# Performance work log

Measured on AMD Instinct MI355X. Metric: run time of the kernel, lower is better.

The kernel has to match this reference:

```python
import jax, jax.numpy as jnp
import numpy as np

B = 4           # batchsize == poolsize, pool = arange(B)
N_NODES = 32768
N_EDGES = 262144
CH_V = 16
CH_E = 16
HID = 64
CH_MSG = 2 * CH_V + CH_E  # 48


def setup_inputs() -> dict:
    key = jax.random.key(0)
    ks = jax.random.split(key, 8)
    node_vals = jax.random.normal(ks[0], (B, N_NODES, CH_V), jnp.float32) * 0.01
    edge_vals = jax.random.normal(ks[1], (B, N_EDGES, CH_E), jnp.float32) * 0.1
    conn_a = jax.random.randint(ks[2], (N_EDGES,), 0, N_NODES)
    conn_b = jax.random.randint(ks[3], (N_EDGES,), 0, N_NODES)
    w = lambda k, sh: jax.random.normal(k, sh, jnp.float32) * 0.1
    return {
        "node_vals": node_vals, "edge_vals": edge_vals,
        "conn_a": conn_a, "conn_b": conn_b,
        "Wm1": w(ks[4], (CH_MSG, HID)), "bm1": jnp.zeros((HID,), jnp.float32),
        "Wm2": w(ks[5], (HID, CH_MSG)), "bm2": jnp.zeros((CH_MSG,), jnp.float32),
        "Wu1": w(ks[6], (3 * CH_V, HID)), "bu1": jnp.zeros((HID,), jnp.float32),
        "Wu2": w(ks[7], (HID, CH_V)), "bu2": jnp.zeros((CH_V,), jnp.float32),
    }


def reference(node_vals, edge_vals, conn_a, conn_b,
              Wm1, bm1, Wm2, bm2, Wu1, bu1, Wu2, bu2):
    # NeuralGraph.timestep with node_dropout_p = edge_dropout_p = 0 (masks are identity),
    # use_update=True, average_messages=True, nodes=True, edges=True.
    h_a = node_vals[:, conn_a]                      # [B, E, CH_V] gather at source nodes
    h_b = node_vals[:, conn_b]                      # [B, E, CH_V] gather at target nodes
    h = jnp.concatenate([h_a, h_b, edge_vals], -1)  # [B, E, 48]
    # message MLP (Linear -> tanh -> Linear)
    m = jnp.tanh(h @ Wm1 + bm1) @ Wm2 + bm2         # [B, E, 48]
    m_a = m[..., :CH_V]
    m_b = m[..., CH_V:2 * CH_V]
    m_ab = m[..., 2 * CH_V:]
    # scatter-add aggregation per node (index_add_ along node dim)
    agg_a = jnp.zeros((B, N_NODES, CH_V), m.dtype).at[:, conn_a].add(m_a)
    agg_b = jnp.zeros((B, N_NODES, CH_V), m.dtype).at[:, conn_b].add(m_b)
    # count-based averaging (counts clamped to >= 1, matching the buffer fixup)
    ones = jnp.ones((N_EDGES,), m.dtype)
    cnt_a = jnp.maximum(jax.ops.segment_sum(ones, conn_a, num_segments=N_NODES), 1.0)
    cnt_b = jnp.maximum(jax.ops.segment_sum(ones, conn_b, num_segments=N_NODES), 1.0)
    agg_a = agg_a / cnt_a[None, :, None]
    agg_b = agg_b / cnt_b[None, :, None]
    # update MLP
    u_in = jnp.concatenate([agg_a, agg_b, node_vals], -1)   # [B, N, 48]
    updates = jnp.tanh(u_in @ Wu1 + bu1) @ Wu2 + bu2        # [B, N, CH_V]
    new_node_vals = node_vals + updates
    new_edge_vals = edge_vals + m_ab
    return new_node_vals, new_edge_vals
```

## Files before the change

kernel.cpp:

```cpp
#include <hip/hip_runtime.h>
#include <hip/hip_bf16.h>
#include <cstdint>
#include <cstddef>

#define B 4
#define NN 32768
#define NE 262144
#define CV 16
#define CE 16
#define HID 64
#define CM 48

using frag  = __attribute__((ext_vector_type(8))) short;
using f32x4 = __attribute__((ext_vector_type(4))) float;

__device__ __forceinline__ float fast_tanh(float x) {
    float e = __expf(2.0f * x);
    return 1.0f - 2.0f / (e + 1.0f);
}

__device__ __forceinline__ unsigned short f2bf(float x) {
    union { float f; unsigned u; } v; v.f = x;
    unsigned r = (v.u + 0x7FFFu + ((v.u >> 16) & 1u)) >> 16;
    return (unsigned short)r;
}

__device__ __forceinline__ float bf2f(unsigned short x) {
    union { unsigned u; float f; } v; v.u = ((unsigned)x) << 16;
    return v.f;
}

__device__ __forceinline__ unsigned pk2bf(float lo, float hi) {
    union { __hip_bfloat162 h; unsigned u; } v;
    v.h = __float22bfloat162_rn(make_float2(lo, hi));
    return v.u;
}

__device__ __forceinline__ unsigned swo(int row, int byte_off) {
    return (unsigned)((row << 7) + (byte_off ^ ((row & 7) << 4)));
}

__device__ __forceinline__ void acc8(float* a, uint4 v) {
    a[0] += bf2f((unsigned short)(v.x & 0xFFFFu));
    a[1] += bf2f((unsigned short)(v.x >> 16));
    a[2] += bf2f((unsigned short)(v.y & 0xFFFFu));
    a[3] += bf2f((unsigned short)(v.y >> 16));
    a[4] += bf2f((unsigned short)(v.z & 0xFFFFu));
    a[5] += bf2f((unsigned short)(v.z >> 16));
    a[6] += bf2f((unsigned short)(v.w & 0xFFFFu));
    a[7] += bf2f((unsigned short)(v.w >> 16));
}

__global__ __launch_bounds__(256) void count_kernel(
    const int* __restrict__ ca, const int* __restrict__ cb,
    int* __restrict__ cnt_a, int* __restrict__ cnt_b,
    int* __restrict__ rank_a, int* __restrict__ rank_b,
    const float* __restrict__ Wm1, const float* __restrict__ bm1,
    const float* __restrict__ Wm2,
    const float* __restrict__ Wu1, const float* __restrict__ bu1,
    const float* __restrict__ Wu2,
    const float* __restrict__ node_vals,
    unsigned short* __restrict__ pW1, unsigned short* __restrict__ pW2,
    unsigned short* __restrict__ pWu1, unsigned short* __restrict__ pWu2,
    unsigned short* __restrict__ nv16)
{
    int i = blockIdx.x * 256 + threadIdx.x;
    rank_a[i] = atomicAdd(&cnt_a[ca[i]], 1);
    rank_b[i] = atomicAdd(&cnt_b[cb[i]], 1);

    {
        int x0 = i * 8;
        const float4* src = (const float4*)(node_vals + x0);
        float4 v0 = src[0], v1 = src[1];
        uint4 o;
        o.x = pk2bf(v0.x, v0.y); o.y = pk2bf(v0.z, v0.w);
        o.z = pk2bf(v1.x, v1.y); o.w = pk2bf(v1.z, v1.w);
        *(uint4*)(nv16 + x0) = o;
    }

    if (blockIdx.x == 0) {
        for (int x = threadIdx.x; x < 4 * 2 * 64 * 8; x += 256) {
            int j = x & 7, lane = (x >> 3) & 63, ks = (x >> 9) & 1, mt = x >> 10;
            int m = mt * 16 + (lane & 15);
            int k = ks * 32 + (lane >> 4) * 8 + j;
            float w = (k < 48) ? Wm1[k * 64 + m] : (k == 48 ? bm1[m] : 0.0f);
            pW1[x] = f2bf(w);
        }
    } else if (blockIdx.x == 1) {
        for (int x = threadIdx.x; x < 3 * 2 * 64 * 8; x += 256) {
            int j = x & 7, lane = (x >> 3) & 63, ks = (x >> 9) & 1, mt = x >> 10;
            int m = mt * 16 + (lane & 15);
            int k = ks * 32 + (lane >> 4) * 8 + j;
            pW2[x] = f2bf(Wm2[k * 48 + m]);
        }
    } else if (blockIdx.x == 2) {
        for (int x = threadIdx.x; x < 4 * 2 * 64 * 8; x += 256) {
            int j = x & 7, lane = (x >> 3) & 63, ks = (x >> 9) & 1, mt = x >> 10;
            int m = mt * 16 + (lane & 15);
            int k = ks * 32 + (lane >> 4) * 8 + j;
            float w = (k < 48) ? Wu1[k * 64 + m] : (k == 48 ? bu1[m] : 0.0f);
            pWu1[x] = f2bf(w);
        }
    } else if (blockIdx.x == 3) {
        for (int x = threadIdx.x; x < 2 * 64 * 8; x += 256) {
            int j = x & 7, lane = (x >> 3) & 63, ks = x >> 9;
            int m = lane & 15;
            int k = ks * 32 + (lane >> 4) * 8 + j;
            pWu2[x] = f2bf(Wu2[k * 16 + m]);
        }
    }
}

__global__ __launch_bounds__(1024) void scan_kernel(
    const int* __restrict__ cnt_a, int* __restrict__ start_a,
    const int* __restrict__ cnt_b, int* __restrict__ start_b)
{
    const int* cnt = (blockIdx.x == 0) ? cnt_a : cnt_b;
    int* start     = (blockIdx.x == 0) ? start_a : start_b;

    __shared__ int sw[16];
    int t = threadIdx.x;
    int lane = t & 63;
    int wv   = t >> 6;
    int base = t * 32;

    int local[32];
    int sum = 0;
    const int4* p = (const int4*)(cnt + base);
#pragma unroll
    for (int q = 0; q < 8; q++) {
        int4 v = p[q];
        local[q*4+0] = v.x; local[q*4+1] = v.y; local[q*4+2] = v.z; local[q*4+3] = v.w;
        sum += v.x + v.y + v.z + v.w;
    }
    int inc = sum;
#pragma unroll
    for (int off = 1; off < 64; off <<= 1) {
        int u = __shfl_up(inc, off);
        if (lane >= off) inc += u;
    }
    if (lane == 63) sw[wv] = inc;
    __syncthreads();
    if (wv == 0 && lane < 16) {
        int v = sw[lane];
        int i2 = v;
#pragma unroll
        for (int off = 1; off < 16; off <<= 1) {
            int u = __shfl_up(i2, off);
            if (lane >= off) i2 += u;
        }
        sw[lane] = i2 - v;
    }
    __syncthreads();

    int run = sw[wv] + inc - sum;
    int4* ps = (int4*)(start + base);
#pragma unroll
    for (int q = 0; q < 8; q++) {
        int4 o;
        o.x = run; run += local[q*4+0];
        o.y = run; run += local[q*4+1];
        o.z = run; run += local[q*4+2];
        o.w = run; run += local[q*4+3];
        ps[q] = o;
    }
}

__global__ __launch_bounds__(256, 5) void edge_kernel(
    const unsigned short* __restrict__ nv16, const float* __restrict__ edge_vals,
    const int* __restrict__ ca, const int* __restrict__ cb,
    const int* __restrict__ rank_a, const int* __restrict__ rank_b,
    const int* __restrict__ start_a, const int* __restrict__ start_b,
    const unsigned short* __restrict__ pW1, const unsigned short* __restrict__ pW2,
    const float* __restrict__ bm2,
    float* __restrict__ out_edge,
    unsigned short* __restrict__ ma_csr, unsigned short* __restrict__ mb_csr)
{
    __shared__ unsigned short sH[256 * 64];
    char* sB = (char*)sH;

    int t    = threadIdx.x;
    int lane = t & 63;
    int col  = lane & 15;
    int quad = lane >> 4;
    int erow = (t >> 6) * 64;

    size_t eb  = (size_t)blockIdx.x * 256;
    size_t idx = eb + t;
    int e  = (int)(idx & (NE - 1));
    int bb = (int)(idx >> 18);

    int na = ca[e], nb = cb[e];
    int posx = start_a[na] + rank_a[e];
    int posy = start_b[nb] + rank_b[e];

    float4 ev[4];
    {
        const uint4* gA = (const uint4*)(nv16 + ((size_t)bb * NN + na) * CV);
        const uint4* gB = (const uint4*)(nv16 + ((size_t)bb * NN + nb) * CV);
        uint4 a0 = gA[0], a1 = gA[1];
        uint4 b0 = gB[0], b1 = gB[1];
        const float4* pE = (const float4*)(edge_vals + idx * CE);
#pragma unroll
        for (int q = 0; q < 4; q++) ev[q] = pE[q];

        unsigned pk[32];
        *(uint4*)&pk[0]  = a0;  *(uint4*)&pk[4]  = a1;
        *(uint4*)&pk[8]  = b0;  *(uint4*)&pk[12] = b1;
#pragma unroll
        for (int q = 0; q < 4; q++) {
            pk[16 + 2*q + 0] = pk2bf(ev[q].x, ev[q].y);
            pk[16 + 2*q + 1] = pk2bf(ev[q].z, ev[q].w);
        }
        pk[24] = 0x3F80u;
#pragma unroll
        for (int q = 25; q < 32; q++) pk[q] = 0;
        const uint4* src = (const uint4*)pk;
#pragma unroll
        for (int q = 0; q < 8; q++)
            *(uint4*)(sB + swo(t, q * 16)) = src[q];
    }
    asm volatile("s_waitcnt lgkmcnt(0)" ::: "memory");

#pragma unroll
    for (int hh = 0; hh < 2; hh++) {
        int r0 = erow + hh * 32 + col;

        frag w1f[4][2];
#pragma unroll
        for (int mt = 0; mt < 4; mt++)
#pragma unroll
            for (int ks = 0; ks < 2; ks++)
                w1f[mt][ks] = *(const frag*)&pW1[(((mt * 2 + ks) * 64) + lane) * 8];

        f32x4 acc1[4][2];
#pragma unroll
        for (int mt = 0; mt < 4; mt++)
#pragma unroll
            for (int n = 0; n < 2; n++) acc1[mt][n] = (f32x4){0.f, 0.f, 0.f, 0.f};

#pragma unroll
        for (int ks = 0; ks < 2; ks++) {
            frag bfr[2];
#pragma unroll
            for (int n = 0; n < 2; n++)
                bfr[n] = *(const frag*)(sB + swo(r0 + n * 16, ks * 64 + quad * 16));
#pragma unroll
            for (int mt = 0; mt < 4; mt++)
#pragma unroll
                for (int n = 0; n < 2; n++)
                    acc1[mt][n] = __builtin_amdgcn_mfma_f32_16x16x32_bf16(
                        w1f[mt][ks], bfr[n], acc1[mt][n], 0, 0, 0);
        }

#pragma unroll
        for (int n = 0; n < 2; n++) {
            int row = r0 + n * 16;
#pragma unroll
            for (int mt = 0; mt < 4; mt++) {
                uint2 w;
                w.x = pk2bf(fast_tanh(acc1[mt][n][0]), fast_tanh(acc1[mt][n][1]));
                w.y = pk2bf(fast_tanh(acc1[mt][n][2]), fast_tanh(acc1[mt][n][3]));
                *(uint2*)(sB + swo(row, mt * 32 + quad * 8)) = w;
            }
        }
        asm volatile("s_waitcnt lgkmcnt(0)" ::: "memory");

        frag w2f[3][2];
#pragma unroll
        for (int mt = 0; mt < 3; mt++)
#pragma unroll
            for (int ks = 0; ks < 2; ks++)
                w2f[mt][ks] = *(const frag*)&pW2[(((mt * 2 + ks) * 64) + lane) * 8];

        f32x4 acc2[3][2];
#pragma unroll
        for (int mt = 0; mt < 3; mt++)
#pragma unroll
            for (int n = 0; n < 2; n++) acc2[mt][n] = (f32x4){0.f, 0.f, 0.f, 0.f};

#pragma unroll
        for (int ks = 0; ks < 2; ks++) {
            frag bfr[2];
#pragma unroll
            for (int n = 0; n < 2; n++)
                bfr[n] = *(const frag*)(sB + swo(r0 + n * 16, ks * 64 + quad * 16));
#pragma unroll
            for (int mt = 0; mt < 3; mt++)
#pragma unroll
                for (int n = 0; n < 2; n++)
                    acc2[mt][n] = __builtin_amdgcn_mfma_f32_16x16x32_bf16(
                        w2f[mt][ks], bfr[n], acc2[mt][n], 0, 0, 0);
        }

#pragma unroll
        for (int n = 0; n < 2; n++) {
            int row = r0 + n * 16;
            float4 v;
            v.x = acc2[2][n][0]; v.y = acc2[2][n][1];
            v.z = acc2[2][n][2]; v.w = acc2[2][n][3];
            *(float4*)(sB + swo(row, 64 + quad * 16)) = v;
        }

        float4 b2a = *(const float4*)&bm2[quad * 4];
        float4 b2b = *(const float4*)&bm2[16 + quad * 4];
#pragma unroll
        for (int n = 0; n < 2; n++) {
            int row = r0 + n * 16;
            uint2 wa;
            wa.x = pk2bf(acc2[0][n][0] + b2a.x, acc2[0][n][1] + b2a.y);
            wa.y = pk2bf(acc2[0][n][2] + b2a.z, acc2[0][n][3] + b2a.w);
            *(uint2*)(sB + swo(row, quad * 8)) = wa;
            uint2 wb;
            wb.x = pk2bf(acc2[1][n][0] + b2b.x, acc2[1][n][1] + b2b.y);
            wb.y = pk2bf(acc2[1][n][2] + b2b.z, acc2[1][n][3] + b2b.w);
            *(uint2*)(sB + swo(row, 32 + quad * 8)) = wb;
        }
    }
    asm volatile("s_waitcnt lgkmcnt(0)" ::: "memory");

    {
        uint4 a0 = *(const uint4*)(sB + swo(t, 0));
        uint4 a1 = *(const uint4*)(sB + swo(t, 16));
        uint4 b0 = *(const uint4*)(sB + swo(t, 32));
        uint4 b1 = *(const uint4*)(sB + swo(t, 48));
        unsigned short* pa = &ma_csr[((size_t)bb * NE + posx) * 16];
        *(uint4*)(pa + 0) = a0;
        *(uint4*)(pa + 8) = a1;
        unsigned short* pb = &mb_csr[((size_t)bb * NE + posy) * 16];
        *(uint4*)(pb + 0) = b0;
        *(uint4*)(pb + 8) = b1;

        const float4* pb2 = (const float4*)&bm2[32];
        float4* po = (float4*)&out_edge[idx * CE];
#pragma unroll
        for (int q = 0; q < 4; q++) {
            float4 m = *(const float4*)(sB + swo(t, 64 + q * 16));
            float4 c = pb2[q];
            float4 o;
            o.x = ev[q].x + m.x + c.x;
            o.y = ev[q].y + m.y + c.y;
            o.z = ev[q].z + m.z + c.z;
            o.w = ev[q].w + m.w + c.w;
            po[q] = o;
        }
    }
}

__global__ __launch_bounds__(256) void node_kernel(
    const float* __restrict__ node_vals,
    const unsigned short* __restrict__ ma_csr, const unsigned short* __restrict__ mb_csr,
    const int* __restrict__ start_a, const int* __restrict__ start_b,
    const int* __restrict__ cnt_a, const int* __restrict__ cnt_b,
    const unsigned short* __restrict__ pWu1, const unsigned short* __restrict__ pWu2,
    const float* __restrict__ bu2,
    float* __restrict__ out_node)
{
    __shared__ unsigned short sH[256 * 64];
    char* sB = (char*)sH;

    int t    = threadIdx.x;
    int lane = t & 63;
    int col  = lane & 15;
    int quad = lane >> 4;
    int erow = (t >> 6) * 64;

    int g = blockIdx.x * 256 + t;
    int n = g & (NN - 1);
    int b = g >> 15;

    float4 pn[4];
    {
        float ua[16] = {0.f,0.f,0.f,0.f,0.f,0.f,0.f,0.f,0.f,0.f,0.f,0.f,0.f,0.f,0.f,0.f};
        float ub[16] = {0.f,0.f,0.f,0.f,0.f,0.f,0.f,0.f,0.f,0.f,0.f,0.f,0.f,0.f,0.f,0.f};
        int da = cnt_a[n], sa = start_a[n];
        int db = cnt_b[n], sbn = start_b[n];
        const unsigned short* pa = ma_csr + ((size_t)b * NE + sa) * 16;
        const unsigned short* pb = mb_csr + ((size_t)b * NE + sbn) * 16;
        for (int k = 0; k < da; k++) {
            acc8(&ua[0], *(const uint4*)(pa + (size_t)k * 16));
            acc8(&ua[8], *(const uint4*)(pa + (size_t)k * 16 + 8));
        }
        for (int k = 0; k < db; k++) {
            acc8(&ub[0], *(const uint4*)(pb + (size_t)k * 16));
            acc8(&ub[8], *(const uint4*)(pb + (size_t)k * 16 + 8));
        }
        float inva = 1.0f / (float)max(da, 1);
        float invb = 1.0f / (float)max(db, 1);

        const float4* pnv = (const float4*)(node_vals + (size_t)g * CV);
#pragma unroll
        for (int q = 0; q < 4; q++) pn[q] = pnv[q];

        unsigned pk[32];
#pragma unroll
        for (int q = 0; q < 8; q++)
            pk[q] = pk2bf(ua[2*q] * inva, ua[2*q+1] * inva);
#pragma unroll
        for (int q = 0; q < 8; q++)
            pk[8 + q] = pk2bf(ub[2*q] * invb, ub[2*q+1] * invb);
#pragma unroll
        for (int q = 0; q < 4; q++) {
            pk[16 + 2*q + 0] = pk2bf(pn[q].x, pn[q].y);
            pk[16 + 2*q + 1] = pk2bf(pn[q].z, pn[q].w);
        }
        pk[24] = 0x3F80u;
#pragma unroll
        for (int q = 25; q < 32; q++) pk[q] = 0;
        const uint4* src = (const uint4*)pk;
#pragma unroll
        for (int q = 0; q < 8; q++)
            *(uint4*)(sB + swo(t, q * 16)) = src[q];
    }
    asm volatile("s_waitcnt lgkmcnt(0)" ::: "memory");

    frag w1f[4][2];
#pragma unroll
    for (int mt = 0; mt < 4; mt++)
#pragma unroll
        for (int ks = 0; ks < 2; ks++)
            w1f[mt][ks] = *(const frag*)&pWu1[(((mt * 2 + ks) * 64) + lane) * 8];

    f32x4 acc1[4][4];
#pragma unroll
    for (int mt = 0; mt < 4; mt++)
#pragma unroll
        for (int nt = 0; nt < 4; nt++) acc1[mt][nt] = (f32x4){0.f, 0.f, 0.f, 0.f};

#pragma unroll
    for (int ks = 0; ks < 2; ks++) {
        frag bfr[4];
#pragma unroll
        for (int nt = 0; nt < 4; nt++)
            bfr[nt] = *(const frag*)(sB + swo(erow + nt*16 + col, ks * 64 + quad * 16));
#pragma unroll
        for (int mt = 0; mt < 4; mt++)
#pragma unroll
            for (int nt = 0; nt < 4; nt++)
                acc1[mt][nt] = __builtin_amdgcn_mfma_f32_16x16x32_bf16(
                    w1f[mt][ks], bfr[nt], acc1[mt][nt], 0, 0, 0);
    }

#pragma unroll
    for (int nt = 0; nt < 4; nt++) {
        int row = erow + nt*16 + col;
#pragma unroll
        for (int mt = 0; mt < 4; mt++) {
            uint2 w;
            w.x = pk2bf(fast_tanh(acc1[mt][nt][0]), fast_tanh(acc1[mt][nt][1]));
            w.y = pk2bf(fast_tanh(acc1[mt][nt][2]), fast_tanh(acc1[mt][nt][3]));
            *(uint2*)(sB + swo(row, mt * 32 + quad * 8)) = w;
        }
    }
    asm volatile("s_waitcnt lgkmcnt(0)" ::: "memory");

    frag w2f[2];
#pragma unroll
    for (int ks = 0; ks < 2; ks++)
        w2f[ks] = *(const frag*)&pWu2[(ks * 64 + lane) * 8];

    f32x4 acc2[4];
#pragma unroll
    for (int nt = 0; nt < 4; nt++) acc2[nt] = (f32x4){0.f, 0.f, 0.f, 0.f};

#pragma unroll
    for (int ks = 0; ks < 2; ks++) {
        frag bfr[4];
#pragma unroll
        for (int nt = 0; nt < 4; nt++)
            bfr[nt] = *(const frag*)(sB + swo(erow + nt*16 + col, ks * 64 + quad * 16));
#pragma unroll
        for (int nt = 0; nt < 4; nt++)
            acc2[nt] = __builtin_amdgcn_mfma_f32_16x16x32_bf16(
                w2f[ks], bfr[nt], acc2[nt], 0, 0, 0);
    }

#pragma unroll
    for (int nt = 0; nt < 4; nt++) {
        int row = erow + nt*16 + col;
        float4 v;
        v.x = acc2[nt][0]; v.y = acc2[nt][1];
        v.z = acc2[nt][2]; v.w = acc2[nt][3];
        *(float4*)(sB + swo(row, quad * 16)) = v;
    }
    asm volatile("s_waitcnt lgkmcnt(0)" ::: "memory");

    {
        const float4* pb2 = (const float4*)bu2;
        float4* po = (float4*)&out_node[(size_t)g * CV];
#pragma unroll
        for (int q = 0; q < 4; q++) {
            float4 m = *(const float4*)(sB + swo(t, q * 16));
            float4 c = pb2[q];
            float4 o;
            o.x = pn[q].x + m.x + c.x;
            o.y = pn[q].y + m.y + c.y;
            o.z = pn[q].z + m.z + c.z;
            o.w = pn[q].w + m.w + c.w;
            po[q] = o;
        }
    }
}

extern "C" void kernel_launch(void* const* d_in, const int* in_sizes, int n_in,
                              void* d_out, int out_size, void* d_ws, size_t ws_size,
                              hipStream_t stream) {
    const float* node_vals = (const float*)d_in[0];
    const float* edge_vals = (const float*)d_in[1];
    const int*   ca        = (const int*)d_in[2];
    const int*   cb        = (const int*)d_in[3];
    const float* Wm1 = (const float*)d_in[4];
    const float* bm1 = (const float*)d_in[5];
    const float* Wm2 = (const float*)d_in[6];
    const float* bm2 = (const float*)d_in[7];
    const float* Wu1 = (const float*)d_in[8];
    const float* bu1 = (const float*)d_in[9];
    const float* Wu2 = (const float*)d_in[10];
    const float* bu2 = (const float*)d_in[11];

    float* out_node = (float*)d_out;
    float* out_edge = out_node + (size_t)B * NN * CV;

    unsigned short* ma_csr = (unsigned short*)d_ws;
    unsigned short* mb_csr = ma_csr + (size_t)B * NE * 16;
    int* cnt_a   = (int*)(mb_csr + (size_t)B * NE * 16);
    int* cnt_b   = cnt_a + NN;
    int* start_a = cnt_b + NN;
    int* start_b = start_a + NN;
    int* rank_a  = start_b + NN;
    int* rank_b  = rank_a + NE;
    unsigned short* pW1  = (unsigned short*)(rank_b + NE);
    unsigned short* pW2  = pW1 + 4096;
    unsigned short* pWu1 = pW2 + 3072;
    unsigned short* pWu2 = pWu1 + 4096;
    unsigned short* nv16 = pWu2 + 1024;

    hipMemsetAsync(cnt_a, 0, 2 * (size_t)NN * sizeof(int), stream);

    count_kernel<<<NE / 256, 256, 0, stream>>>(
        ca, cb, cnt_a, cnt_b, rank_a, rank_b,
        Wm1, bm1, Wm2, Wu1, bu1, Wu2, node_vals,
        pW1, pW2, pWu1, pWu2, nv16);
    scan_kernel<<<2, 1024, 0, stream>>>(cnt_a, start_a, cnt_b, start_b);
    edge_kernel<<<(B * NE) / 256, 256, 0, stream>>>(
        nv16, edge_vals, ca, cb, rank_a, rank_b, start_a, start_b,
        pW1, pW2, bm2, out_edge, ma_csr, mb_csr);
    node_kernel<<<(B * NN) / 256, 256, 0, stream>>>(
        node_vals, ma_csr, mb_csr, start_a, start_b, cnt_a, cnt_b,
        pWu1, pWu2, bu2, out_node);
}
```

Baseline: 312.8 us.

## Store messages in edge order and gather via CSR edge-index lists

The edge kernel now writes per-edge messages contiguously in edge order instead of scattering them into CSR-permuted positions, and a new small kernel builds per-node edge-index lists. The node kernel then gathers messages indirectly through those index lists. The edge-output residual is also written straight from MFMA accumulators, re-reading edge_vals rather than staging through shared memory. This trades scattered writes for scattered reads plus an extra index load and an extra kernel launch, and it holds fewer registers across the MLP.

```diff
diff --git a/kernel.cpp b/kernel.cpp
--- a/kernel.cpp
+++ b/kernel.cpp
@@ -166,15 +166,24 @@
     }
 }
 
+__global__ __launch_bounds__(256) void eidx_kernel(
+    const int* __restrict__ ca, const int* __restrict__ cb,
+    const int* __restrict__ rank_a, const int* __restrict__ rank_b,
+    const int* __restrict__ start_a, const int* __restrict__ start_b,
+    int* __restrict__ eidx_a, int* __restrict__ eidx_b)
+{
+    int e = blockIdx.x * 256 + threadIdx.x;
+    eidx_a[start_a[ca[e]] + rank_a[e]] = e;
+    eidx_b[start_b[cb[e]] + rank_b[e]] = e;
+}
+
 __global__ __launch_bounds__(256, 5) void edge_kernel(
     const unsigned short* __restrict__ nv16, const float* __restrict__ edge_vals,
     const int* __restrict__ ca, const int* __restrict__ cb,
-    const int* __restrict__ rank_a, const int* __restrict__ rank_b,
-    const int* __restrict__ start_a, const int* __restrict__ start_b,
     const unsigned short* __restrict__ pW1, const unsigned short* __restrict__ pW2,
     const float* __restrict__ bm2,
     float* __restrict__ out_edge,
-    unsigned short* __restrict__ ma_csr, unsigned short* __restrict__ mb_csr)
+    unsigned short* __restrict__ ma, unsigned short* __restrict__ mb)
 {
     __shared__ unsigned short sH[256 * 64];
     char* sB = (char*)sH;
@@ -184,6 +193,7 @@
     int col  = lane & 15;
     int quad = lane >> 4;
     int erow = (t >> 6) * 64;
+    int cha  = quad * 4;
 
     size_t eb  = (size_t)blockIdx.x * 256;
     size_t idx = eb + t;
@@ -191,27 +201,22 @@
     int bb = (int)(idx >> 18);
 
     int na = ca[e], nb = cb[e];
-    int posx = start_a[na] + rank_a[e];
-    int posy = start_b[nb] + rank_b[e];
-
-    float4 ev[4];
+
     {
         const uint4* gA = (const uint4*)(nv16 + ((size_t)bb * NN + na) * CV);
         const uint4* gB = (const uint4*)(nv16 + ((size_t)bb * NN + nb) * CV);
         uint4 a0 = gA[0], a1 = gA[1];
         uint4 b0 = gB[0], b1 = gB[1];
         const float4* pE = (const float4*)(edge_vals + idx * CE);
-#pragma unroll
-        for (int q = 0; q < 4; q++) ev[q] = pE[q];
+        float4 ev0 = pE[0], ev1 = pE[1], ev2 = pE[2], ev3 = pE[3];
 
         unsigned pk[32];
         *(uint4*)&pk[0]  = a0;  *(uint4*)&pk[4]  = a1;
         *(uint4*)&pk[8]  = b0;  *(uint4*)&pk[12] = b1;
-#pragma unroll
-        for (int q = 0; q < 4; q++) {
-            pk[16 + 2*q + 0] = pk2bf(ev[q].x, ev[q].y);
-            pk[16 + 2*q + 1] = pk2bf(ev[q].z, ev[q].w);
-        }
+        pk[16] = pk2bf(ev0.x, ev0.y); pk[17] = pk2bf(ev0.z, ev0.w);
+        pk[18] = pk2bf(ev1.x, ev1.y); pk[19] = pk2bf(ev1.z, ev1.w);
+        pk[20] = pk2bf(ev2.x, ev2.y); pk[21] = pk2bf(ev2.z, ev2.w);
+        pk[22] = pk2bf(ev3.x, ev3.y); pk[23] = pk2bf(ev3.z, ev3.w);
         pk[24] = 0x3F80u;
 #pragma unroll
         for (int q = 25; q < 32; q++) pk[q] = 0;
@@ -293,17 +298,22 @@
                         w2f[mt][ks], bfr[n], acc2[mt][n], 0, 0, 0);
         }
 
+        float4 b2e = *(const float4*)&bm2[32 + cha];
 #pragma unroll
         for (int n = 0; n < 2; n++) {
-            int row = r0 + n * 16;
-            float4 v;
-            v.x = acc2[2][n][0]; v.y = acc2[2][n][1];
-            v.z = acc2[2][n][2]; v.w = acc2[2][n][3];
-            *(float4*)(sB + swo(row, 64 + quad * 16)) = v;
-        }
-
-        float4 b2a = *(const float4*)&bm2[quad * 4];
-        float4 b2b = *(const float4*)&bm2[16 + quad * 4];
+            int le = r0 + n * 16;
+            size_t o = (eb + le) * CE + cha;
+            float4 evv = *(const float4*)&edge_vals[o];
+            float4 ov;
+            ov.x = evv.x + acc2[2][n][0] + b2e.x;
+            ov.y = evv.y + acc2[2][n][1] + b2e.y;
+            ov.z = evv.z + acc2[2][n][2] + b2e.z;
+            ov.w = evv.w + acc2[2][n][3] + b2e.w;
+            *(float4*)&out_edge[o] = ov;
+        }
+
+        float4 b2a = *(const float4*)&bm2[cha];
+        float4 b2b = *(const float4*)&bm2[16 + cha];
 #pragma unroll
         for (int n = 0; n < 2; n++) {
             int row = r0 + n * 16;
@@ -324,32 +334,19 @@
         uint4 a1 = *(const uint4*)(sB + swo(t, 16));
         uint4 b0 = *(const uint4*)(sB + swo(t, 32));
         uint4 b1 = *(const uint4*)(sB + swo(t, 48));
-        unsigned short* pa = &ma_csr[((size_t)bb * NE + posx) * 16];
+        unsigned short* pa = &ma[idx * 16];
         *(uint4*)(pa + 0) = a0;
         *(uint4*)(pa + 8) = a1;
-        unsigned short* pb = &mb_csr[((size_t)bb * NE + posy) * 16];
+        unsigned short* pb = &mb[idx * 16];
         *(uint4*)(pb + 0) = b0;
         *(uint4*)(pb + 8) = b1;
-
-        const float4* pb2 = (const float4*)&bm2[32];
-        float4* po = (float4*)&out_edge[idx * CE];
-#pragma unroll
-        for (int q = 0; q < 4; q++) {
-            float4 m = *(const float4*)(sB + swo(t, 64 + q * 16));
-            float4 c = pb2[q];
-            float4 o;
-            o.x = ev[q].x + m.x + c.x;
-            o.y = ev[q].y + m.y + c.y;
-            o.z = ev[q].z + m.z + c.z;
-            o.w = ev[q].w + m.w + c.w;
-            po[q] = o;
-        }
     }
 }
 
 __global__ __launch_bounds__(256) void node_kernel(
     const float* __restrict__ node_vals,
-    const unsigned short* __restrict__ ma_csr, const unsigned short* __restrict__ mb_csr,
+    const unsigned short* __restrict__ ma, const unsigned short* __restrict__ mb,
+    const int* __restrict__ eidx_a, const int* __restrict__ eidx_b,
     const int* __restrict__ start_a, const int* __restrict__ start_b,
     const int* __restrict__ cnt_a, const int* __restrict__ cnt_b,
     const unsigned short* __restrict__ pWu1, const unsigned short* __restrict__ pWu2,
@@ -375,15 +372,21 @@
         float ub[16] = {0.f,0.f,0.f,0.f,0.f,0.f,0.f,0.f,0.f,0.f,0.f,0.f,0.f,0.f,0.f,0.f};
         int da = cnt_a[n], sa = start_a[n];
         int db = cnt_b[n], sbn = start_b[n];
-        const unsigned short* pa = ma_csr + ((size_t)b * NE + sa) * 16;
-        const unsigned short* pb = mb_csr + ((size_t)b * NE + sbn) * 16;
+        const int* ia = eidx_a + sa;
+        const int* ib = eidx_b + sbn;
+        const unsigned short* mab = ma + (size_t)b * NE * 16;
+        const unsigned short* mbb = mb + (size_t)b * NE * 16;
         for (int k = 0; k < da; k++) {
-            acc8(&ua[0], *(const uint4*)(pa + (size_t)k * 16));
-            acc8(&ua[8], *(const uint4*)(pa + (size_t)k * 16 + 8));
+            int ee = ia[k];
+            const uint4* p = (const uint4*)(mab + (size_t)ee * 16);
+            acc8(&ua[0], p[0]);
+            acc8(&ua[8], p[1]);
         }
         for (int k = 0; k < db; k++) {
-            acc8(&ub[0], *(const uint4*)(pb + (size_t)k * 16));
-            acc8(&ub[8], *(const uint4*)(pb + (size_t)k * 16 + 8));
+            int ee = ib[k];
+            const uint4* p = (const uint4*)(mbb + (size_t)ee * 16);
+            acc8(&ub[0], p[0]);
+            acc8(&ub[8], p[1]);
         }
         float inva = 1.0f / (float)max(da, 1);
         float invb = 1.0f / (float)max(db, 1);
@@ -521,15 +524,17 @@
     float* out_node = (float*)d_out;
     float* out_edge = out_node + (size_t)B * NN * CV;
 
-    unsigned short* ma_csr = (unsigned short*)d_ws;
-    unsigned short* mb_csr = ma_csr + (size_t)B * NE * 16;
-    int* cnt_a   = (int*)(mb_csr + (size_t)B * NE * 16);
+    unsigned short* ma = (unsigned short*)d_ws;
+    unsigned short* mb = ma + (size_t)B * NE * 16;
+    int* cnt_a   = (int*)(mb + (size_t)B * NE * 16);
     int* cnt_b   = cnt_a + NN;
     int* start_a = cnt_b + NN;
     int* start_b = start_a + NN;
     int* rank_a  = start_b + NN;
     int* rank_b  = rank_a + NE;
-    unsigned short* pW1  = (unsigned short*)(rank_b + NE);
+    int* eidx_a  = rank_b + NE;
+    int* eidx_b  = eidx_a + NE;
+    unsigned short* pW1  = (unsigned short*)(eidx_b + NE);
     unsigned short* pW2  = pW1 + 4096;
     unsigned short* pWu1 = pW2 + 3072;
     unsigned short* pWu2 = pWu1 + 4096;
@@ -542,10 +547,11 @@
         Wm1, bm1, Wm2, Wu1, bu1, Wu2, node_vals,
         pW1, pW2, pWu1, pWu2, nv16);
     scan_kernel<<<2, 1024, 0, stream>>>(cnt_a, start_a, cnt_b, start_b);
+    eidx_kernel<<<NE / 256, 256, 0, stream>>>(
+        ca, cb, rank_a, rank_b, start_a, start_b, eidx_a, eidx_b);
     edge_kernel<<<(B * NE) / 256, 256, 0, stream>>>(
-        nv16, edge_vals, ca, cb, rank_a, rank_b, start_a, start_b,
-        pW1, pW2, bm2, out_edge, ma_csr, mb_csr);
+        nv16, edge_vals, ca, cb, pW1, pW2, bm2, out_edge, ma, mb);
     node_kernel<<<(B * NN) / 256, 256, 0, stream>>>(
-        node_vals, ma_csr, mb_csr, start_a, start_b, cnt_a, cnt_b,
+        node_vals, ma, mb, eidx_a, eidx_b, start_a, start_b, cnt_a, cnt_b,
         pWu1, pWu2, bu2, out_node);
 }
```

After: 282.8 us. -9.6%, faster.
